# Kernel tuning notes

Hardware: AMD Instinct MI355X
Metric: run time of the kernel (lower is better)

Reference implementation:

```python
import jax, jax.numpy as jnp
import numpy as np

# Synthetic layered DAG: 8 node-layers of width N -> 7 masked dense layers.
B = 4096        # batch
N = 2048        # nodes per DAG layer (= in_features = out_features)
DEPTH = 7       # number of weight layers (len(L) - 1)
DENSITY = 0.25  # fraction of predecessor edges present (mask sparsity)


def setup_inputs() -> dict:
    key = jax.random.key(0)
    kx, kw, km = jax.random.split(key, 3)
    x = jax.random.normal(kx, (B, N), dtype=jnp.float32)
    # Mask M: [DEPTH, N+1, N]; random 0/1 edges, last row (bias) all ones.
    m = (jax.random.uniform(km, (DEPTH, N + 1, N)) < DENSITY).astype(jnp.float32)
    M = m.at[:, -1, :].set(1.0)
    # Kaiming-uniform per column: bound = 1/sqrt(nnz_j) (torch code's init),
    # nonzero only at masked positions (W initialized to zeros elsewhere).
    nnz = jnp.maximum(M.sum(axis=1, keepdims=True), 1.0)  # [DEPTH,1,N]
    u = jax.random.uniform(kw, (DEPTH, N + 1, N), minval=-1.0, maxval=1.0)
    W = (u / jnp.sqrt(nnz)) * M
    return {"x": x, "W": W, "M": M}


def reference(x, W, M):
    # activations buffer semantics collapse to a per-layer chain because each
    # layer's preds are exactly the previous DAG layer; sinks = last layer.
    def step(acts, wm):
        w, m = wm  # [N+1, N] each
        h = jnp.concatenate(
            [acts, jnp.ones((acts.shape[0], 1), acts.dtype)], axis=1)  # [B, N+1]
        acts = jax.nn.relu(h @ (m * w))  # masked dense matmul + ReLU
        return acts, None

    out, _ = jax.lax.scan(step, x, (W, M))
    return out  # [B, N] activations of sink nodes
```

## Files before the change

### kernel.cpp

```cpp
#include <hip/hip_runtime.h>
#include <hip/hip_bf16.h>

typedef __bf16 bf16_t;
typedef __bf16 v8bf __attribute__((ext_vector_type(8)));
typedef __bf16 v4bf __attribute__((ext_vector_type(4)));
typedef float  v4f  __attribute__((ext_vector_type(4)));

#define B_ROWS 4096
#define N_COLS 2048
#define K_FULL 2049
#define K_PAD  2176
#define DEPTH  7

#define BM 128
#define BN 128
#define BK 128
#define NT (K_PAD / BK)

__global__ __launch_bounds__(256) void wt_kernel(const float* __restrict__ W,
                                                 bf16_t* __restrict__ Wt) {
  __shared__ float t[64][65];
  const int l  = blockIdx.z;
  const int k0 = blockIdx.x * 64;
  const int n0 = blockIdx.y * 64;
  const int tid = threadIdx.x;
  const int r  = tid >> 4;
  const int c4 = (tid & 15) * 4;
  const float* Wl = W + (size_t)l * K_FULL * N_COLS;
#pragma unroll
  for (int it = 0; it < 4; ++it) {
    const int k = k0 + r + it * 16;
    float4 v = make_float4(0.f, 0.f, 0.f, 0.f);
    if (k < K_FULL) v = *(const float4*)&Wl[(size_t)k * N_COLS + n0 + c4];
    t[c4 + 0][r + it * 16] = v.x;
    t[c4 + 1][r + it * 16] = v.y;
    t[c4 + 2][r + it * 16] = v.z;
    t[c4 + 3][r + it * 16] = v.w;
  }
  __syncthreads();
  bf16_t* Wtl = Wt + (size_t)l * N_COLS * K_PAD;
#pragma unroll
  for (int it = 0; it < 4; ++it) {
    const int n = r + it * 16;
    v4bf o;
    o[0] = (bf16_t)t[n][c4 + 0];
    o[1] = (bf16_t)t[n][c4 + 1];
    o[2] = (bf16_t)t[n][c4 + 2];
    o[3] = (bf16_t)t[n][c4 + 3];
    *(v4bf*)&Wtl[(size_t)(n0 + n) * K_PAD + k0 + c4] = o;
  }
}

__global__ __launch_bounds__(256) void init_kernel(const float* __restrict__ x,
                                                   bf16_t* __restrict__ A0,
                                                   bf16_t* __restrict__ A1) {
  const int c4 = (blockIdx.x * 256 + threadIdx.x) * 4;
  const int r  = blockIdx.y;
  if (c4 >= K_PAD) return;
  v4bf o;
  if (c4 < N_COLS) {
    const float4 v = *(const float4*)&x[(size_t)r * N_COLS + c4];
    o[0] = (bf16_t)v.x; o[1] = (bf16_t)v.y; o[2] = (bf16_t)v.z; o[3] = (bf16_t)v.w;
  } else {
    o[0] = (bf16_t)(c4 == N_COLS ? 1.0f : 0.0f);
    o[1] = (bf16_t)0.0f; o[2] = (bf16_t)0.0f; o[3] = (bf16_t)0.0f;
  }
  *(v4bf*)&A0[(size_t)r * K_PAD + c4] = o;
  if (c4 >= N_COLS) *(v4bf*)&A1[(size_t)r * K_PAD + c4] = o;
}

__global__ __launch_bounds__(512, 4) void gemm_kernel(
    const bf16_t* __restrict__ A, const bf16_t* __restrict__ Bt,
    bf16_t* __restrict__ Cn, float* __restrict__ Co) {
  __shared__ __align__(16) bf16_t As[BM * BK];
  __shared__ __align__(16) bf16_t Bs[BN * BK];

  const int tid  = threadIdx.x;
  const int wave = tid >> 6;
  const int lane = tid & 63;
  const int m0 = blockIdx.y * BM;
  const int n0 = blockIdx.x * BN;
  const int wm = (wave & 1) * 64;
  const int wn = (wave >> 1) * 32;
  const int quad = lane >> 4;
  const int l16  = lane & 15;

  int srow[4], scol[4];
#pragma unroll
  for (int c = 0; c < 4; ++c) {
    const int gran = wave * 256 + c * 64 + lane;
    srow[c] = gran >> 4;
    scol[c] = ((gran & 15) ^ (srow[c] & 15)) << 3;
  }
  size_t aoff[4], boff[4];
#pragma unroll
  for (int c = 0; c < 4; ++c) {
    aoff[c] = (size_t)(m0 + srow[c]) * K_PAD + scol[c];
    boff[c] = (size_t)(n0 + srow[c]) * K_PAD + scol[c];
  }

  v4f acc[4][2] = {};

  for (int kt = 0; kt < NT; ++kt) {
    const int kbase = kt * BK;
    __syncthreads();
#pragma unroll
    for (int c = 0; c < 4; ++c) {
      __builtin_amdgcn_global_load_lds(
          (const __attribute__((address_space(1))) void*)(A + aoff[c] + kbase),
          (__attribute__((address_space(3))) void*)((char*)As + wave * 4096 + c * 1024),
          16, 0, 0);
    }
#pragma unroll
    for (int c = 0; c < 4; ++c) {
      __builtin_amdgcn_global_load_lds(
          (const __attribute__((address_space(1))) void*)(Bt + boff[c] + kbase),
          (__attribute__((address_space(3))) void*)((char*)Bs + wave * 4096 + c * 1024),
          16, 0, 0);
    }
    __syncthreads();

#pragma unroll
    for (int ks = 0; ks < 4; ++ks) {
      v8bf af[4], bfr[2];
      const int kg = ks * 4 + quad;
#pragma unroll
      for (int i = 0; i < 4; ++i) {
        const int arow = wm + i * 16 + l16;
        af[i] = *(const v8bf*)&As[arow * BK + ((kg ^ (arow & 15)) << 3)];
      }
#pragma unroll
      for (int j = 0; j < 2; ++j) {
        const int brow = wn + j * 16 + l16;
        bfr[j] = *(const v8bf*)&Bs[brow * BK + ((kg ^ (brow & 15)) << 3)];
      }
#pragma unroll
      for (int i = 0; i < 4; ++i)
#pragma unroll
        for (int j = 0; j < 2; ++j)
          acc[i][j] = __builtin_amdgcn_mfma_f32_16x16x32_bf16(af[i], bfr[j],
                                                              acc[i][j], 0, 0, 0);
    }
  }

#pragma unroll
  for (int i = 0; i < 4; ++i) {
#pragma unroll
    for (int j = 0; j < 2; ++j) {
#pragma unroll
      for (int r = 0; r < 4; ++r) {
        float v = acc[i][j][r];
        v = v > 0.0f ? v : 0.0f;
        const int row = m0 + wm + i * 16 + quad * 4 + r;
        const int col = n0 + wn + j * 16 + l16;
        if (Co) Co[(size_t)row * N_COLS + col] = v;
        else    Cn[(size_t)row * K_PAD + col] = (bf16_t)v;
      }
    }
  }
}

extern "C" void kernel_launch(void* const* d_in, const int* in_sizes, int n_in,
                              void* d_out, int out_size, void* d_ws, size_t ws_size,
                              hipStream_t stream) {
  const float* x = (const float*)d_in[0];
  const float* W = (const float*)d_in[1];
  float* out = (float*)d_out;

  char* ws = (char*)d_ws;
  const size_t wtBytes = (size_t)DEPTH * N_COLS * K_PAD * sizeof(bf16_t);
  const size_t aBytes  = (size_t)B_ROWS * K_PAD * sizeof(bf16_t);
  bf16_t* Wt = (bf16_t*)ws;
  bf16_t* A0 = (bf16_t*)(ws + wtBytes);
  bf16_t* A1 = (bf16_t*)(ws + wtBytes + aBytes);

  wt_kernel<<<dim3(K_PAD / 64, N_COLS / 64, DEPTH), 256, 0, stream>>>(W, Wt);
  init_kernel<<<dim3((K_PAD / 4 + 255) / 256, B_ROWS), 256, 0, stream>>>(x, A0, A1);

  bf16_t* bufs[2] = {A0, A1};
  for (int l = 0; l < DEPTH; ++l) {
    const bf16_t* Ain = bufs[l & 1];
    bf16_t* Aout      = bufs[(l + 1) & 1];
    const bf16_t* Bl  = Wt + (size_t)l * N_COLS * K_PAD;
    const bool last   = (l == DEPTH - 1);
    gemm_kernel<<<dim3(N_COLS / BN, B_ROWS / BM), 512, 0, stream>>>(
        Ain, Bl, last ? nullptr : Aout, last ? out : nullptr);
  }
}
```

Baseline: 505.0 us.

## Double-buffer LDS tiles with BK=64 and use 4 waves each computing 64x64

The GEMM now uses two LDS buffers with a K-tile of 64 and issues the global-to-LDS loads for the next tile before computing on the current one, so memory traffic overlaps MFMA work. The block shrinks from 8 waves to 4, and each wave computes a 64x64 sub-tile (16 accumulators) instead of 64x32. The swizzle changes to an 8-granule XOR to match the narrower tile. This raises register use per wave and relies on a single barrier per iteration for correctness of the double buffer. Offsets are now 32-bit ints.

```diff
diff --git a/kernel.cpp b/kernel.cpp
--- a/kernel.cpp
+++ b/kernel.cpp
@@ -14,7 +14,7 @@
 
 #define BM 128
 #define BN 128
-#define BK 128
+#define BK 64
 #define NT (K_PAD / BK)
 
 __global__ __launch_bounds__(256) void wt_kernel(const float* __restrict__ W,
@@ -69,11 +69,11 @@
   if (c4 >= N_COLS) *(v4bf*)&A1[(size_t)r * K_PAD + c4] = o;
 }
 
-__global__ __launch_bounds__(512, 4) void gemm_kernel(
+__global__ __launch_bounds__(256, 2) void gemm_kernel(
     const bf16_t* __restrict__ A, const bf16_t* __restrict__ Bt,
     bf16_t* __restrict__ Cn, float* __restrict__ Co) {
-  __shared__ __align__(16) bf16_t As[BM * BK];
-  __shared__ __align__(16) bf16_t Bs[BN * BK];
+  __shared__ __align__(16) bf16_t As[2][BM * BK];
+  __shared__ __align__(16) bf16_t Bs[2][BN * BK];
 
   const int tid  = threadIdx.x;
   const int wave = tid >> 6;
@@ -81,72 +81,75 @@
   const int m0 = blockIdx.y * BM;
   const int n0 = blockIdx.x * BN;
   const int wm = (wave & 1) * 64;
-  const int wn = (wave >> 1) * 32;
+  const int wn = (wave >> 1) * 64;
   const int quad = lane >> 4;
   const int l16  = lane & 15;
 
-  int srow[4], scol[4];
+  int aoff[4], boff[4];
 #pragma unroll
   for (int c = 0; c < 4; ++c) {
     const int gran = wave * 256 + c * 64 + lane;
-    srow[c] = gran >> 4;
-    scol[c] = ((gran & 15) ^ (srow[c] & 15)) << 3;
-  }
-  size_t aoff[4], boff[4];
-#pragma unroll
-  for (int c = 0; c < 4; ++c) {
-    aoff[c] = (size_t)(m0 + srow[c]) * K_PAD + scol[c];
-    boff[c] = (size_t)(n0 + srow[c]) * K_PAD + scol[c];
+    const int srow = gran >> 3;
+    const int scol = ((gran & 7) ^ (srow & 7)) << 3;
+    aoff[c] = (m0 + srow) * K_PAD + scol;
+    boff[c] = (n0 + srow) * K_PAD + scol;
   }
 
-  v4f acc[4][2] = {};
-
-  for (int kt = 0; kt < NT; ++kt) {
-    const int kbase = kt * BK;
-    __syncthreads();
+  auto stage = [&](int buf, int kb) {
 #pragma unroll
     for (int c = 0; c < 4; ++c) {
       __builtin_amdgcn_global_load_lds(
-          (const __attribute__((address_space(1))) void*)(A + aoff[c] + kbase),
-          (__attribute__((address_space(3))) void*)((char*)As + wave * 4096 + c * 1024),
+          (const __attribute__((address_space(1))) void*)(A + aoff[c] + kb),
+          (__attribute__((address_space(3))) void*)((char*)&As[buf][0] + wave * 4096 + c * 1024),
           16, 0, 0);
     }
 #pragma unroll
     for (int c = 0; c < 4; ++c) {
       __builtin_amdgcn_global_load_lds(
-          (const __attribute__((address_space(1))) void*)(Bt + boff[c] + kbase),
-          (__attribute__((address_space(3))) void*)((char*)Bs + wave * 4096 + c * 1024),
+          (const __attribute__((address_space(1))) void*)(Bt + boff[c] + kb),
+          (__attribute__((address_space(3))) void*)((char*)&Bs[buf][0] + wave * 4096 + c * 1024),
           16, 0, 0);
     }
-    __syncthreads();
+  };
+
+  v4f acc[4][4] = {};
+
+  stage(0, 0);
+  __syncthreads();
+
+#pragma unroll 2
+  for (int kt = 0; kt < NT; ++kt) {
+    const int cur = kt & 1;
+    if (kt + 1 < NT) stage(cur ^ 1, (kt + 1) * BK);
 
 #pragma unroll
-    for (int ks = 0; ks < 4; ++ks) {
-      v8bf af[4], bfr[2];
+    for (int ks = 0; ks < 2; ++ks) {
+      v8bf af[4], bfr[4];
       const int kg = ks * 4 + quad;
 #pragma unroll
       for (int i = 0; i < 4; ++i) {
         const int arow = wm + i * 16 + l16;
-        af[i] = *(const v8bf*)&As[arow * BK + ((kg ^ (arow & 15)) << 3)];
+        af[i] = *(const v8bf*)&As[cur][arow * BK + ((kg ^ (arow & 7)) << 3)];
       }
 #pragma unroll
-      for (int j = 0; j < 2; ++j) {
+      for (int j = 0; j < 4; ++j) {
         const int brow = wn + j * 16 + l16;
-        bfr[j] = *(const v8bf*)&Bs[brow * BK + ((kg ^ (brow & 15)) << 3)];
+        bfr[j] = *(const v8bf*)&Bs[cur][brow * BK + ((kg ^ (brow & 7)) << 3)];
       }
 #pragma unroll
       for (int i = 0; i < 4; ++i)
 #pragma unroll
-        for (int j = 0; j < 2; ++j)
+        for (int j = 0; j < 4; ++j)
           acc[i][j] = __builtin_amdgcn_mfma_f32_16x16x32_bf16(af[i], bfr[j],
                                                               acc[i][j], 0, 0, 0);
     }
+    __syncthreads();
   }
 
 #pragma unroll
   for (int i = 0; i < 4; ++i) {
 #pragma unroll
-    for (int j = 0; j < 2; ++j) {
+    for (int j = 0; j < 4; ++j) {
 #pragma unroll
       for (int r = 0; r < 4; ++r) {
         float v = acc[i][j][r];
@@ -183,7 +186,7 @@
     bf16_t* Aout      = bufs[(l + 1) & 1];
     const bf16_t* Bl  = Wt + (size_t)l * N_COLS * K_PAD;
     const bool last   = (l == DEPTH - 1);
-    gemm_kernel<<<dim3(N_COLS / BN, B_ROWS / BM), 512, 0, stream>>>(
+    gemm_kernel<<<dim3(N_COLS / BN, B_ROWS / BM), 256, 0, stream>>>(
         Ain, Bl, last ? nullptr : Aout, last ? out : nullptr);
   }
 }
```

New measurement: 541.3 us. 1.07x slower.

## Drop padded bias K-tile, add fp32 bias in epilogue, swizzle block order

Applied to the files above, without the earlier changes.

Shrinks the GEMM reduction from a padded K of 2176 to exactly 2048 by pulling the bias row out of the weight matrix and adding it as an fp32 vector in the epilogue. This removes one of seventeen K tiles per layer and the padded activation columns. The grid becomes a 1D launch with a remapped block order meant to improve L2 reuse of the A and B tiles. Offsets now use 32-bit ints, which is safe at these sizes. The bias is also added in fp32 rather than bf16, which slightly changes the numerics.

```diff
diff --git a/kernel.cpp b/kernel.cpp
--- a/kernel.cpp
+++ b/kernel.cpp
@@ -9,13 +9,13 @@
 #define B_ROWS 4096
 #define N_COLS 2048
 #define K_FULL 2049
-#define K_PAD  2176
+#define KK     2048
 #define DEPTH  7
 
 #define BM 128
 #define BN 128
 #define BK 128
-#define NT (K_PAD / BK)
+#define NKT (KK / BK)
 
 __global__ __launch_bounds__(256) void wt_kernel(const float* __restrict__ W,
                                                  bf16_t* __restrict__ Wt) {
@@ -30,15 +30,14 @@
 #pragma unroll
   for (int it = 0; it < 4; ++it) {
     const int k = k0 + r + it * 16;
-    float4 v = make_float4(0.f, 0.f, 0.f, 0.f);
-    if (k < K_FULL) v = *(const float4*)&Wl[(size_t)k * N_COLS + n0 + c4];
+    const float4 v = *(const float4*)&Wl[(size_t)k * N_COLS + n0 + c4];
     t[c4 + 0][r + it * 16] = v.x;
     t[c4 + 1][r + it * 16] = v.y;
     t[c4 + 2][r + it * 16] = v.z;
     t[c4 + 3][r + it * 16] = v.w;
   }
   __syncthreads();
-  bf16_t* Wtl = Wt + (size_t)l * N_COLS * K_PAD;
+  bf16_t* Wtl = Wt + (size_t)l * N_COLS * KK;
 #pragma unroll
   for (int it = 0; it < 4; ++it) {
     const int n = r + it * 16;
@@ -47,61 +46,65 @@
     o[1] = (bf16_t)t[n][c4 + 1];
     o[2] = (bf16_t)t[n][c4 + 2];
     o[3] = (bf16_t)t[n][c4 + 3];
-    *(v4bf*)&Wtl[(size_t)(n0 + n) * K_PAD + k0 + c4] = o;
+    *(v4bf*)&Wtl[(size_t)(n0 + n) * KK + k0 + c4] = o;
   }
 }
 
+__global__ __launch_bounds__(256) void bias_kernel(const float* __restrict__ W,
+                                                   float* __restrict__ Bias) {
+  const int i = (blockIdx.x * 256 + threadIdx.x) * 4;
+  if (i >= DEPTH * N_COLS) return;
+  const int l = i >> 11;
+  const int n = i & (N_COLS - 1);
+  *(float4*)&Bias[i] =
+      *(const float4*)&W[(size_t)l * K_FULL * N_COLS + (size_t)KK * N_COLS + n];
+}
+
 __global__ __launch_bounds__(256) void init_kernel(const float* __restrict__ x,
-                                                   bf16_t* __restrict__ A0,
-                                                   bf16_t* __restrict__ A1) {
+                                                   bf16_t* __restrict__ A0) {
   const int c4 = (blockIdx.x * 256 + threadIdx.x) * 4;
   const int r  = blockIdx.y;
-  if (c4 >= K_PAD) return;
+  const float4 v = *(const float4*)&x[(size_t)r * N_COLS + c4];
   v4bf o;
-  if (c4 < N_COLS) {
-    const float4 v = *(const float4*)&x[(size_t)r * N_COLS + c4];
-    o[0] = (bf16_t)v.x; o[1] = (bf16_t)v.y; o[2] = (bf16_t)v.z; o[3] = (bf16_t)v.w;
-  } else {
-    o[0] = (bf16_t)(c4 == N_COLS ? 1.0f : 0.0f);
-    o[1] = (bf16_t)0.0f; o[2] = (bf16_t)0.0f; o[3] = (bf16_t)0.0f;
-  }
-  *(v4bf*)&A0[(size_t)r * K_PAD + c4] = o;
-  if (c4 >= N_COLS) *(v4bf*)&A1[(size_t)r * K_PAD + c4] = o;
+  o[0] = (bf16_t)v.x; o[1] = (bf16_t)v.y; o[2] = (bf16_t)v.z; o[3] = (bf16_t)v.w;
+  *(v4bf*)&A0[(size_t)r * N_COLS + c4] = o;
 }
 
 __global__ __launch_bounds__(512, 4) void gemm_kernel(
     const bf16_t* __restrict__ A, const bf16_t* __restrict__ Bt,
+    const float* __restrict__ bias,
     bf16_t* __restrict__ Cn, float* __restrict__ Co) {
   __shared__ __align__(16) bf16_t As[BM * BK];
   __shared__ __align__(16) bf16_t Bs[BN * BK];
 
+  const int bid = blockIdx.x;
+  const int swz = (bid & 7) * 64 + (bid >> 3);
+  const int bx  = swz & 15;
+  const int by  = swz >> 4;
+
   const int tid  = threadIdx.x;
   const int wave = tid >> 6;
   const int lane = tid & 63;
-  const int m0 = blockIdx.y * BM;
-  const int n0 = blockIdx.x * BN;
+  const int m0 = by * BM;
+  const int n0 = bx * BN;
   const int wm = (wave & 1) * 64;
   const int wn = (wave >> 1) * 32;
   const int quad = lane >> 4;
   const int l16  = lane & 15;
 
-  int srow[4], scol[4];
+  int aoff[4], boff[4];
 #pragma unroll
   for (int c = 0; c < 4; ++c) {
     const int gran = wave * 256 + c * 64 + lane;
-    srow[c] = gran >> 4;
-    scol[c] = ((gran & 15) ^ (srow[c] & 15)) << 3;
-  }
-  size_t aoff[4], boff[4];
-#pragma unroll
-  for (int c = 0; c < 4; ++c) {
-    aoff[c] = (size_t)(m0 + srow[c]) * K_PAD + scol[c];
-    boff[c] = (size_t)(n0 + srow[c]) * K_PAD + scol[c];
+    const int srow = gran >> 4;
+    const int scol = ((gran & 15) ^ (srow & 15)) << 3;
+    aoff[c] = (m0 + srow) * KK + scol;
+    boff[c] = (n0 + srow) * KK + scol;
   }
 
   v4f acc[4][2] = {};
 
-  for (int kt = 0; kt < NT; ++kt) {
+  for (int kt = 0; kt < NKT; ++kt) {
     const int kbase = kt * BK;
     __syncthreads();
 #pragma unroll
@@ -143,18 +146,21 @@
     }
   }
 
+  float bv[2];
+#pragma unroll
+  for (int j = 0; j < 2; ++j) bv[j] = bias[n0 + wn + j * 16 + l16];
 #pragma unroll
   for (int i = 0; i < 4; ++i) {
 #pragma unroll
     for (int j = 0; j < 2; ++j) {
 #pragma unroll
       for (int r = 0; r < 4; ++r) {
-        float v = acc[i][j][r];
+        float v = acc[i][j][r] + bv[j];
         v = v > 0.0f ? v : 0.0f;
         const int row = m0 + wm + i * 16 + quad * 4 + r;
         const int col = n0 + wn + j * 16 + l16;
         if (Co) Co[(size_t)row * N_COLS + col] = v;
-        else    Cn[(size_t)row * K_PAD + col] = (bf16_t)v;
+        else    Cn[(size_t)row * N_COLS + col] = (bf16_t)v;
       }
     }
   }
@@ -168,22 +174,25 @@
   float* out = (float*)d_out;
 
   char* ws = (char*)d_ws;
-  const size_t wtBytes = (size_t)DEPTH * N_COLS * K_PAD * sizeof(bf16_t);
-  const size_t aBytes  = (size_t)B_ROWS * K_PAD * sizeof(bf16_t);
-  bf16_t* Wt = (bf16_t*)ws;
-  bf16_t* A0 = (bf16_t*)(ws + wtBytes);
-  bf16_t* A1 = (bf16_t*)(ws + wtBytes + aBytes);
+  const size_t wtBytes = (size_t)DEPTH * N_COLS * KK * sizeof(bf16_t);
+  const size_t aBytes  = (size_t)B_ROWS * N_COLS * sizeof(bf16_t);
+  bf16_t* Wt   = (bf16_t*)ws;
+  bf16_t* A0   = (bf16_t*)(ws + wtBytes);
+  bf16_t* A1   = (bf16_t*)(ws + wtBytes + aBytes);
+  float*  Bias = (float*)(ws + wtBytes + 2 * aBytes);
 
-  wt_kernel<<<dim3(K_PAD / 64, N_COLS / 64, DEPTH), 256, 0, stream>>>(W, Wt);
-  init_kernel<<<dim3((K_PAD / 4 + 255) / 256, B_ROWS), 256, 0, stream>>>(x, A0, A1);
+  wt_kernel<<<dim3(KK / 64, N_COLS / 64, DEPTH), 256, 0, stream>>>(W, Wt);
+  bias_kernel<<<dim3((DEPTH * N_COLS / 4 + 255) / 256), 256, 0, stream>>>(W, Bias);
+  init_kernel<<<dim3(N_COLS / 4 / 256, B_ROWS), 256, 0, stream>>>(x, A0);
 
   bf16_t* bufs[2] = {A0, A1};
   for (int l = 0; l < DEPTH; ++l) {
     const bf16_t* Ain = bufs[l & 1];
     bf16_t* Aout      = bufs[(l + 1) & 1];
-    const bf16_t* Bl  = Wt + (size_t)l * N_COLS * K_PAD;
+    const bf16_t* Bl  = Wt + (size_t)l * N_COLS * KK;
+    const float* bl   = Bias + (size_t)l * N_COLS;
     const bool last   = (l == DEPTH - 1);
-    gemm_kernel<<<dim3(N_COLS / BN, B_ROWS / BM), 512, 0, stream>>>(
-        Ain, Bl, last ? nullptr : Aout, last ? out : nullptr);
+    gemm_kernel<<<dim3((B_ROWS / BM) * (N_COLS / BN)), 512, 0, stream>>>(
+        Ain, Bl, bl, last ? nullptr : Aout, last ? out : nullptr);
   }
 }
```

New measurement: 478.9 us. -5.2%, faster.
